# Kernel optimization log

Hardware: AMD Instinct MI355X
Metric: run time of the kernel (lower is better)

Reference implementation:

```python
import jax, jax.numpy as jnp
import numpy as np
from jax import lax

BN_EPS = 1e-5


def _fps(xyz, npoint):
    # Farthest point sampling; deterministic start at index 0 per batch
    # (original uses a random start; the math of the loop is identical).
    B, N, _ = xyz.shape
    init_dist = jnp.full((B, N), 1e10, dtype=xyz.dtype)
    init_far = jnp.zeros((B,), dtype=jnp.int32)

    def step(carry, _):
        dist, far = carry
        centroid = jnp.take_along_axis(xyz, far[:, None, None], axis=1)  # [B,1,3]
        d = jnp.sum((xyz - centroid) ** 2, axis=-1)  # [B,N]
        dist = jnp.minimum(dist, d)
        new_far = jnp.argmax(dist, axis=-1).astype(jnp.int32)
        return (dist, new_far), far

    _, idx = lax.scan(step, (init_dist, init_far), None, length=npoint)
    return jnp.transpose(idx)  # [B, npoint]


def _index_points(points, idx):
    # points [B,N,C], idx [B,...] -> [B,...,C]
    return jax.vmap(lambda p, i: p[i])(points, idx)


def _knn(k, xyz, new_xyz):
    # squared euclidean distances [B,S,N]
    d = (jnp.sum(new_xyz ** 2, -1)[:, :, None]
         + jnp.sum(xyz ** 2, -1)[:, None, :]
         - 2.0 * jnp.einsum('bsc,bnc->bsn', new_xyz, xyz))
    _, idx = lax.top_k(-d, k)  # k smallest distances
    return idx


def _conv_bn_relu(x, w, gamma, beta):
    # 1x1 Conv2d (no bias) + BatchNorm2d (training-mode batch stats) + ReLU
    y = jnp.einsum('oc,bcsk->bosk', w, x)
    mean = jnp.mean(y, axis=(0, 2, 3), keepdims=True)
    var = jnp.var(y, axis=(0, 2, 3), keepdims=True)
    y = (y - mean) * lax.rsqrt(var + BN_EPS)
    y = y * gamma[None, :, None, None] + beta[None, :, None, None]
    return jax.nn.relu(y)


def setup_inputs() -> dict:
    key = jax.random.key(0)
    ks = jax.random.split(key, 5)
    B, N, C = 16, 4096, 128
    xyz = jax.random.normal(ks[0], (B, N, 3), dtype=jnp.float32)
    features = jax.random.normal(ks[1], (B, C, N), dtype=jnp.float32)
    w1 = jax.random.normal(ks[2], (128, C + 3), dtype=jnp.float32) * 0.05
    w2 = jax.random.normal(ks[3], (128, 128), dtype=jnp.float32) * 0.05
    w3 = jax.random.normal(ks[4], (256, 128), dtype=jnp.float32) * 0.05
    return {
        'xyz': xyz, 'features': features,
        'w1': w1, 'g1': jnp.ones(128), 'b1': jnp.zeros(128),
        'w2': w2, 'g2': jnp.ones(128), 'b2': jnp.zeros(128),
        'w3': w3, 'g3': jnp.ones(256), 'b3': jnp.zeros(256),
        'npoint': 1024, 'k': 32,
    }


def reference(xyz, features, w1, g1, b1, w2, g2, b2, w3, g3, b3, npoint, k):
    fps_idx = _fps(xyz, npoint)                     # [B,S]
    new_xyz = _index_points(xyz, fps_idx)           # [B,S,3]
    group_idx = _knn(k, xyz, new_xyz)               # [B,S,K]
    grouped_xyz = _index_points(xyz, group_idx)     # [B,S,K,3]
    gxn = grouped_xyz - new_xyz[:, :, None, :]
    feats = jnp.transpose(features, (0, 2, 1))      # [B,N,C]
    gfeat = _index_points(feats, group_idx)         # [B,S,K,C]
    grouped = jnp.concatenate([gxn, gfeat], axis=-1)  # [B,S,K,3+C]
    x = jnp.transpose(grouped, (0, 3, 1, 2))        # [B,3+C,S,K]
    x = _conv_bn_relu(x, w1, g1, b1)
    x = _conv_bn_relu(x, w2, g2, b2)
    x = _conv_bn_relu(x, w3, g3, b3)
    new_features = jnp.max(x, axis=-1)              # [B,256,S]
    return new_xyz, new_features
```

## Files before the change

### kernel.cpp

```cpp
#include <hip/hip_runtime.h>

#define HB 16
#define HN 4096
#define HS 1024
#define HK 32
#define HC 128

typedef _Float16 half8  __attribute__((ext_vector_type(8)));
typedef _Float16 half4v __attribute__((ext_vector_type(4)));
typedef float    f32x4  __attribute__((ext_vector_type(4)));
typedef float    f32x2  __attribute__((ext_vector_type(2)));
typedef unsigned long long u64;

#define WS_BN      4096u
#define WS_A1H     8192u
#define WS_A2H     49152u
#define WS_A3H     81920u
#define WS_XYZPP   147456u
#define WS_GIDX    1196032u
#define WS_FEATT   3293184u
#define WS_Y1      20070400u

__global__ __launch_bounds__(256) void head_kernel(
    const float* __restrict__ xyz, const float* __restrict__ features,
    const float* __restrict__ w1, const float* __restrict__ w2, const float* __restrict__ w3,
    _Float16* __restrict__ a1h, _Float16* __restrict__ a2h, _Float16* __restrict__ a3h,
    _Float16* __restrict__ featt, float4* __restrict__ xyzpp, float* __restrict__ out)
{
#pragma clang fp contract(off)
  __shared__ union {
    float tbuf[64][65];
    struct {
      float xyzt[HN*3];
      unsigned long long K[2][4];
    } fps;
  } lds;
  const int bid = blockIdx.x;
  const int t = threadIdx.x;

  if (bid < 16) {
    const int b = bid;
    const float* xb = xyz + (size_t)b*HN*3;
    f32x2 pX[8], pY[8], pZ[8], dm[8];
    #pragma unroll
    for (int h = 0; h < 8; ++h) {
      #pragma unroll
      for (int e = 0; e < 2; ++e) {
        int n = t*16 + h*2 + e;
        float x = xb[n*3+0], y = xb[n*3+1], z = xb[n*3+2];
        pX[h][e] = x; pY[h][e] = y; pZ[h][e] = z;
        lds.fps.xyzt[n*3+0] = x; lds.fps.xyzt[n*3+1] = y; lds.fps.xyzt[n*3+2] = z;
      }
      dm[h] = f32x2{1e10f, 1e10f};
    }
    float cx = xb[0], cy = xb[1], cz = xb[2];
    float sc[4][3];
    #pragma unroll
    for (int k = 0; k < 4; ++k) { sc[k][0]=0.0f; sc[k][1]=0.0f; sc[k][2]=0.0f; }
    if (t == 0) { out[(size_t)(b*HS)*3+0] = cx; out[(size_t)(b*HS)*3+1] = cy; out[(size_t)(b*HS)*3+2] = cz; }
    const int wv = t >> 6, l = t & 63;

    for (int i = 1; i < HS; ++i) {
      f32x2 vcx = {cx, cx}, vcy = {cy, cy}, vcz = {cz, cz};
      float pm[8];
      #pragma unroll
      for (int h = 0; h < 8; ++h) {
        f32x2 dx = pX[h] - vcx, dy = pY[h] - vcy, dz = pZ[h] - vcz;
        f32x2 d = ((dx*dx) + (dy*dy)) + (dz*dz);
        f32x2 nd = __builtin_elementwise_min(dm[h], d);
        dm[h] = nd;
        pm[h] = fmaxf(nd[0], nd[1]);
      }
      float q0 = fmaxf(pm[0], pm[1]), q1 = fmaxf(pm[2], pm[3]);
      float q2 = fmaxf(pm[4], pm[5]), q3 = fmaxf(pm[6], pm[7]);
      float mymax = fmaxf(fmaxf(q0, q1), fmaxf(q2, q3));
      int xk = __float_as_int(mymax);
      #define WMAXSTEP(ctrl) { int o_ = __builtin_amdgcn_update_dpp(xk, xk, ctrl, 0xF, 0xF, false); \
        xk = __float_as_int(fmaxf(__int_as_float(xk), __int_as_float(o_))); }
      WMAXSTEP(0x111) WMAXSTEP(0x112) WMAXSTEP(0x114)
      WMAXSTEP(0x118) WMAXSTEP(0x142) WMAXSTEP(0x143)
      #undef WMAXSTEP
      float wmax = __int_as_float(__builtin_amdgcn_readlane(xk, 63));
      unsigned long long msk = __ballot(mymax == wmax);
      int winl = __ffsll(msk) - 1;
      int j = 0;
      #pragma unroll
      for (int h = 7; h >= 0; --h) {
        int e = (dm[h][0] == wmax) ? 0 : 1;
        if (pm[h] == wmax) j = 2*h + e;
      }
      int n_cand = t*16 + j;
      int n_w = __builtin_amdgcn_readlane(n_cand, winl);

      const int p = i & 1;
      if (l == 0) {
        lds.fps.K[p][wv] = ((unsigned long long)__float_as_uint(wmax) << 32)
                         | (unsigned int)(HN-1 - n_w);
      }
      __syncthreads();
      unsigned long long k0 = lds.fps.K[p][0], k1 = lds.fps.K[p][1];
      unsigned long long k2 = lds.fps.K[p][2], k3 = lds.fps.K[p][3];
      unsigned long long ka = (k0 >= k1) ? k0 : k1;
      unsigned long long kb = (k2 >= k3) ? k2 : k3;
      unsigned long long kk = (ka >= kb) ? ka : kb;
      int n_best = HN-1 - (int)(unsigned int)(kk & 0xFFFFFFFFull);
      int off = n_best*3;
      cx = lds.fps.xyzt[off+0];
      cy = lds.fps.xyzt[off+1];
      cz = lds.fps.xyzt[off+2];
      if ((i & 255) == t) {
        int s = i >> 8;
        #pragma unroll
        for (int k = 0; k < 4; ++k)
          if (s == k) { sc[k][0] = cx; sc[k][1] = cy; sc[k][2] = cz; }
      }
    }
    #pragma unroll
    for (int k = 0; k < 4; ++k) {
      int i = k*256 + t;
      if (i >= 1) {
        size_t o3 = (size_t)(b*HS + i)*3;
        out[o3+0] = sc[k][0]; out[o3+1] = sc[k][1]; out[o3+2] = sc[k][2];
      }
    }
  } else if (bid < 16 + 1024) {
    const int tb = bid - 16;
    const int bb = tb >> 6, n0 = (tb & 63) * 64;
    const int wvv = t >> 6, lane = t & 63;
    for (int h = 0; h < 2; ++h) {
      #pragma unroll
      for (int rep = 0; rep < 16; ++rep) {
        int cc = rep*4 + wvv;
        lds.tbuf[cc][lane] = features[((size_t)(bb*HC + h*64 + cc))*HN + n0 + lane];
      }
      __syncthreads();
      #pragma unroll
      for (int rep = 0; rep < 2; ++rep) {
        int item = rep*256 + t;
        int n = item >> 3, cg = (item & 7) * 8;
        half8 v;
        #pragma unroll
        for (int j = 0; j < 8; ++j) v[j] = (_Float16)lds.tbuf[cg + j][n];
        *(half8*)(featt + ((size_t)(bb*HN) + n0 + n) * HC + h*64 + cg) = v;
      }
      __syncthreads();
    }
  } else if (bid < 16 + 1024 + 256) {
    int gi = (bid - 1040)*256 + t;
    const float* p = xyz + (size_t)gi*3;
    float x = p[0], y = p[1], z = p[2];
    float pp = ((x*x) + (y*y)) + (z*z);
    xyzpp[gi] = make_float4(x, y, z, pp);
  } else {
    int wi = (bid - 1296)*256 + t;
    if (wi < 20480) {
      int o = wi / 160, c = wi - o*160;
      float v = 0.0f;
      if (c < 128) v = w1[o*131 + 3 + c];
      else if (c < 131) v = w1[o*131 + (c-128)];
      a1h[wi] = (_Float16)v;
    } else if (wi < 20480 + 16384) {
      a2h[wi - 20480] = (_Float16)w2[wi - 20480];
    } else if (wi < 20480 + 16384 + 32768) {
      a3h[wi - 36864] = (_Float16)w3[wi - 36864];
    }
  }
}

#define LEXLT(d1,i1,d2,i2) ((d1) < (d2) || ((d1) == (d2) && (i1) < (i2)))

__global__ __launch_bounds__(64) void knn_p1(
    const float* __restrict__ newxyz, const float4* __restrict__ xyzpp, u64* __restrict__ keybuf)
{
#pragma clang fp contract(off)
  const int t = threadIdx.x;
  const int blk = blockIdx.x;
  const int b = blk >> 7, rem = blk & 127;
  const int shard = rem >> 4, qg = rem & 15;
  const int q = b*1024 + qg*64 + t;
  float qx = newxyz[(size_t)q*3+0], qy = newxyz[(size_t)q*3+1], qz = newxyz[(size_t)q*3+2];
  float qq = ((qx*qx) + (qy*qy)) + (qz*qz);

  const float INF = __builtin_inff();
  float td[32]; int ti[32];
  #pragma unroll
  for (int j = 0; j < 32; ++j) { td[j] = INF; ti[j] = 0x7FFFFFFF; }
  float root = INF;
  int cnt = 0;

  __shared__ float fdl[32][64];
  __shared__ int   fil[32][64];
  const float4* P = xyzpp + (size_t)b*HN + shard*512;

  auto flush = [&]() {
    float gd[32]; int gi2[32];
    #pragma unroll
    for (int j = 0; j < 32; ++j) {
      gd[j] = fdl[j][t]; gi2[j] = fil[j][t];
      if (j >= cnt) { gd[j] = INF; gi2[j] = 0x7FFFFFFF; }
    }
    cnt = 0;
    #pragma unroll
    for (int k = 2; k <= 32; k <<= 1) {
      #pragma unroll
      for (int j = k >> 1; j > 0; j >>= 1) {
        #pragma unroll
        for (int i = 0; i < 32; ++i) {
          int l = i ^ j;
          if (l > i) {
            bool up = ((i & k) == 0);
            bool sw = up ? LEXLT(gd[l], gi2[l], gd[i], gi2[i])
                         : LEXLT(gd[i], gi2[i], gd[l], gi2[l]);
            if (sw) { float tf = gd[i]; gd[i] = gd[l]; gd[l] = tf;
                      int   ii = gi2[i]; gi2[i] = gi2[l]; gi2[l] = ii; }
          }
        }
      }
    }
    #pragma unroll
    for (int i = 0; i < 32; ++i) {
      float od = gd[31-i]; int oi = gi2[31-i];
      if (LEXLT(od, oi, td[i], ti[i])) { td[i] = od; ti[i] = oi; }
    }
    #pragma unroll
    for (int j = 16; j > 0; j >>= 1) {
      #pragma unroll
      for (int i = 0; i < 32; ++i) {
        if ((i & j) == 0) {
          int l = i | j;
          if (LEXLT(td[l], ti[l], td[i], ti[i])) {
            float tf = td[i]; td[i] = td[l]; td[l] = tf;
            int   ii = ti[i]; ti[i] = ti[l]; ti[l] = ii;
          }
        }
      }
    }
    root = td[31];
  };

  for (int n0 = 0; n0 < 512; n0 += 8) {
    float4 pb[8];
    #pragma unroll
    for (int j = 0; j < 8; ++j) pb[j] = P[n0 + j];
    #pragma unroll
    for (int j = 0; j < 8; ++j) {
      float d = (qq + pb[j].w) - 2.0f*(((qx*pb[j].x) + (qy*pb[j].y)) + (qz*pb[j].z));
      if (d < root) { fdl[cnt][t] = d; fil[cnt][t] = shard*512 + n0 + j; cnt++; }
    }
    if (__ballot(cnt > 24)) flush();
  }
  if (__ballot(cnt > 0)) flush();

  const size_t base = (size_t)(b*16 + qg) * 16384 + (size_t)shard * 2048;
  #pragma unroll
  for (int j = 0; j < 32; ++j) {
    unsigned bits = __float_as_uint(td[j]);
    unsigned s = bits ^ (((unsigned)((int)bits >> 31)) | 0x80000000u);
    keybuf[base + (size_t)j*64 + t] = ((u64)s << 32) | (unsigned)ti[j];
  }
}

__global__ __launch_bounds__(64) void knn_p2(const u64* __restrict__ keybuf, int* __restrict__ gidx)
{
  const int t = threadIdx.x;
  const int g = blockIdx.x;
  const size_t base = (size_t)g * 16384;

  u64 tk[32];
  #pragma unroll
  for (int j = 0; j < 32; ++j) tk[j] = ~0ULL;
  u64 root = ~0ULL;
  int cnt = 0;
  __shared__ u64 fk[32][64];

  auto flush64 = [&]() {
    u64 gd[32];
    #pragma unroll
    for (int j = 0; j < 32; ++j) {
      gd[j] = fk[j][t];
      if (j >= cnt) gd[j] = ~0ULL;
    }
    cnt = 0;
    #pragma unroll
    for (int k = 2; k <= 32; k <<= 1) {
      #pragma unroll
      for (int j = k >> 1; j > 0; j >>= 1) {
        #pragma unroll
        for (int i = 0; i < 32; ++i) {
          int l = i ^ j;
          if (l > i) {
            bool up = ((i & k) == 0);
            bool sw = up ? (gd[l] < gd[i]) : (gd[i] < gd[l]);
            if (sw) { u64 tf = gd[i]; gd[i] = gd[l]; gd[l] = tf; }
          }
        }
      }
    }
    #pragma unroll
    for (int i = 0; i < 32; ++i) {
      u64 od = gd[31-i];
      if (od < tk[i]) tk[i] = od;
    }
    #pragma unroll
    for (int j = 16; j > 0; j >>= 1) {
      #pragma unroll
      for (int i = 0; i < 32; ++i) {
        if ((i & j) == 0) {
          int l = i | j;
          if (tk[l] < tk[i]) { u64 tf = tk[i]; tk[i] = tk[l]; tk[l] = tf; }
        }
      }
    }
    root = tk[31];
  };

  for (int k0 = 0; k0 < 256; k0 += 8) {
    u64 kk[8];
    #pragma unroll
    for (int j = 0; j < 8; ++j) kk[j] = keybuf[base + (size_t)(k0 + j)*64 + t];
    #pragma unroll
    for (int j = 0; j < 8; ++j) {
      if (kk[j] < root) { fk[cnt][t] = kk[j]; cnt++; }
    }
    if (__ballot(cnt > 24)) flush64();
  }
  if (__ballot(cnt > 0)) flush64();

  const int q = g*64 + t;
  #pragma unroll
  for (int j = 0; j < 32; j += 4) {
    int4 v = { (int)(unsigned)tk[j], (int)(unsigned)tk[j+1], (int)(unsigned)tk[j+2], (int)(unsigned)tk[j+3] };
    *(int4*)(gidx + ((size_t)q << 5) + j) = v;
  }
}

template<int MODE>
__global__ __launch_bounds__(256, 2) void conv_kernel(
    const _Float16* __restrict__ A, const _Float16* Bsrc,
    const int* __restrict__ gidx, const float4* __restrict__ xyzpp, const float* __restrict__ newxyz,
    const _Float16* __restrict__ bnA, const _Float16* __restrict__ bnB,
    _Float16* Yout, float* __restrict__ pstat, float* __restrict__ pool)
{
  const int tid = threadIdx.x;
  const int w = tid >> 6, l = tid & 63, ll = l & 15, lh = l >> 4;
  const int colbase = blockIdx.x * 256 + w * 64;
  const int b = colbase >> 15;
  const int AS = (MODE == 1) ? 160 : 128;
  const _Float16* Ap = A + (MODE == 3 ? (size_t)blockIdx.y * 128 * 128 : 0);

  f32x4 acc[8][4] = {};

  half8 bnAv[4], bnBv[4];
  if constexpr (MODE >= 2) {
    #pragma unroll
    for (int c = 0; c < 4; ++c) {
      int k0 = c*32 + lh*8;
      bnAv[c] = *(const half8*)(bnA + k0);
      bnBv[c] = *(const half8*)(bnB + k0);
    }
  }
  int gidxv[4];
  if constexpr (MODE == 1) {
    #pragma unroll
    for (int nf = 0; nf < 4; ++nf) gidxv[nf] = gidx[colbase + nf*16 + ll];
  }

  const int NCH = (MODE == 1) ? 5 : 4;
  #pragma unroll
  for (int c = 0; c < NCH; ++c) {
    half8 a[8];
    #pragma unroll
    for (int mf = 0; mf < 8; ++mf)
      a[mf] = *(const half8*)(Ap + (size_t)(mf*16 + ll)*AS + c*32 + lh*8);
    half8 bfr[4];
    #pragma unroll
    for (int nf = 0; nf < 4; ++nf) {
      if constexpr (MODE == 1) {
        if (c < 4) {
          bfr[nf] = *(const half8*)(Bsrc + ((size_t)(b*HN + gidxv[nf]))*HC + c*32 + lh*8);
        } else {
          half8 z = {};
          if (lh == 0) {
            float4 pw = xyzpp[b*HN + gidxv[nf]];
            int col = colbase + nf*16 + ll;
            int s = (col >> 5) & (HS-1);
            const float* nx = newxyz + (size_t)(b*HS + s)*3;
            z[0] = (_Float16)(pw.x - nx[0]);
            z[1] = (_Float16)(pw.y - nx[1]);
            z[2] = (_Float16)(pw.z - nx[2]);
          }
          bfr[nf] = z;
        }
      } else {
        half8 v = *(const half8*)(Bsrc + ((size_t)(colbase + nf*16 + ll))*HC + c*32 + lh*8);
        v = v * bnAv[c] + bnBv[c];
        half8 hz = {};
        bfr[nf] = __builtin_elementwise_max(v, hz);
      }
    }
    #pragma unroll
    for (int mf = 0; mf < 8; ++mf)
      #pragma unroll
      for (int nf = 0; nf < 4; ++nf)
        acc[mf][nf] = __builtin_amdgcn_mfma_f32_16x16x32_f16(a[mf], bfr[nf], acc[mf][nf], 0, 0, 0);
  }

  __shared__ float bsum[128], bsq[128];
  if (tid < 128) { bsum[tid] = 0.0f; bsq[tid] = 0.0f; }
  __syncthreads();

  #pragma unroll
  for (int mf = 0; mf < 8; ++mf) {
    int ch0 = mf*16 + lh*4;
    if constexpr (MODE != 3) {
      #pragma unroll
      for (int nf = 0; nf < 4; ++nf) {
        int col = colbase + nf*16 + ll;
        half4v hv;
        #pragma unroll
        for (int r = 0; r < 4; ++r) hv[r] = (_Float16)acc[mf][nf][r];
        *(half4v*)(Yout + (size_t)col*HC + ch0) = hv;
      }
    } else {
      #pragma unroll
      for (int g = 0; g < 2; ++g) {
        float mx[4];
        #pragma unroll
        for (int r = 0; r < 4; ++r) mx[r] = fmaxf(acc[mf][2*g][r], acc[mf][2*g+1][r]);
        #pragma unroll
        for (int m = 1; m <= 8; m <<= 1)
          #pragma unroll
          for (int r = 0; r < 4; ++r) mx[r] = fmaxf(mx[r], __shfl_xor(mx[r], m, 64));
        if (ll == 0) {
          int s = ((colbase + g*32) >> 5) & (HS-1);
          int chg = blockIdx.y*128 + ch0;
          #pragma unroll
          for (int r = 0; r < 4; ++r)
            pool[(((size_t)(b*256 + chg + r)) << 10) + s] = mx[r];
        }
      }
    }
    float sv[4] = {0,0,0,0}, qv[4] = {0,0,0,0};
    #pragma unroll
    for (int nf = 0; nf < 4; ++nf)
      #pragma unroll
      for (int r = 0; r < 4; ++r) { float v = acc[mf][nf][r]; sv[r] += v; qv[r] += v*v; }
    #pragma unroll
    for (int m = 1; m <= 8; m <<= 1)
      #pragma unroll
      for (int r = 0; r < 4; ++r) { sv[r] += __shfl_xor(sv[r], m, 64); qv[r] += __shfl_xor(qv[r], m, 64); }
    if (ll == 0) {
      #pragma unroll
      for (int r = 0; r < 4; ++r) { atomicAdd(&bsum[ch0+r], sv[r]); atomicAdd(&bsq[ch0+r], qv[r]); }
    }
  }
  __syncthreads();
  float pv = (tid < 128) ? bsum[tid] : bsq[tid - 128];
  pstat[((size_t)(blockIdx.y * gridDim.x + blockIdx.x)) * 256 + tid] = pv;
}

__global__ __launch_bounds__(256) void fin_kernel(
    const float* __restrict__ pstat, int nblk,
    const float* __restrict__ g, const float* __restrict__ be,
    _Float16* __restrict__ Ah, _Float16* __restrict__ Bh,
    float* __restrict__ Af, float* __restrict__ Bf)
{
  const int ch = blockIdx.x;
  const int y = ch >> 7, c = ch & 127;
  const float* base = pstat + (size_t)y * nblk * 256;
  const int t = threadIdx.x;
  float s = 0.0f, q = 0.0f;
  for (int k = t; k < nblk; k += 256) {
    s += base[(size_t)k*256 + c];
    q += base[(size_t)k*256 + 128 + c];
  }
  #pragma unroll
  for (int m = 1; m < 64; m <<= 1) { s += __shfl_xor(s, m, 64); q += __shfl_xor(q, m, 64); }
  __shared__ float ss[4], sq[4];
  if ((t & 63) == 0) { ss[t >> 6] = s; sq[t >> 6] = q; }
  __syncthreads();
  if (t == 0) {
    s = ((ss[0] + ss[1]) + (ss[2] + ss[3]));
    q = ((sq[0] + sq[1]) + (sq[2] + sq[3]));
    float mean = s * (1.0f/524288.0f);
    float var  = q * (1.0f/524288.0f) - mean*mean;
    float a  = g[ch] * rsqrtf(var + 1e-5f);
    float bb = be[ch] - mean*a;
    if (Ah) { Ah[ch] = (_Float16)a; Bh[ch] = (_Float16)bb; }
    else    { Af[ch] = a; Bf[ch] = bb; }
  }
}

__global__ __launch_bounds__(256) void final_affine(float* __restrict__ outp,
                                                    const float* __restrict__ Af,
                                                    const float* __restrict__ Bf)
{
  int i = blockIdx.x*256 + threadIdx.x;
  float4 v = ((float4*)outp)[i];
  int ch = ((i << 2) >> 10) & 255;
  float a = Af[ch], bb = Bf[ch];
  v.x = fmaxf(v.x*a + bb, 0.0f);
  v.y = fmaxf(v.y*a + bb, 0.0f);
  v.z = fmaxf(v.z*a + bb, 0.0f);
  v.w = fmaxf(v.w*a + bb, 0.0f);
  ((float4*)outp)[i] = v;
}

extern "C" void kernel_launch(void* const* d_in, const int* in_sizes, int n_in,
                              void* d_out, int out_size, void* d_ws, size_t ws_size,
                              hipStream_t stream) {
  const float* xyz      = (const float*)d_in[0];
  const float* features = (const float*)d_in[1];
  const float* w1  = (const float*)d_in[2];
  const float* g1  = (const float*)d_in[3];
  const float* b1v = (const float*)d_in[4];
  const float* w2  = (const float*)d_in[5];
  const float* g2  = (const float*)d_in[6];
  const float* b2v = (const float*)d_in[7];
  const float* w3  = (const float*)d_in[8];
  const float* g3  = (const float*)d_in[9];
  const float* b3v = (const float*)d_in[10];
  float* out = (float*)d_out;
  char* ws = (char*)d_ws;

  _Float16* A1h = (_Float16*)(ws + WS_BN);
  _Float16* B1h = A1h + 128;
  _Float16* A2h = A1h + 256;
  _Float16* B2h = A1h + 384;
  float* a3f = (float*)(ws + WS_BN + 1024);
  float* b3f = a3f + 256;
  _Float16* a1h = (_Float16*)(ws + WS_A1H);
  _Float16* a2h = (_Float16*)(ws + WS_A2H);
  _Float16* a3h = (_Float16*)(ws + WS_A3H);
  float4* xyzpp = (float4*)(ws + WS_XYZPP);
  int* gidx = (int*)(ws + WS_GIDX);
  _Float16* featt = (_Float16*)(ws + WS_FEATT);
  u64* keybuf = (u64*)(ws + WS_Y1);
  _Float16* y1 = (_Float16*)(ws + WS_Y1);
  _Float16* y2 = y1;

  float* p1 = out + 49152;
  float* p2 = (float*)(ws + WS_FEATT);
  float* p3 = (float*)(ws + WS_FEATT + 4194304);

  head_kernel<<<1568, 256, 0, stream>>>(xyz, features, w1, w2, w3,
                                        a1h, a2h, a3h, featt, xyzpp, out);
  knn_p1<<<2048, 64, 0, stream>>>(out, xyzpp, keybuf);
  knn_p2<<<256, 64, 0, stream>>>(keybuf, gidx);

  conv_kernel<1><<<2048, 256, 0, stream>>>(a1h, featt, gidx, xyzpp, out,
                                           nullptr, nullptr, y1, p1, nullptr);
  fin_kernel<<<128, 256, 0, stream>>>(p1, 2048, g1, b1v, A1h, B1h, nullptr, nullptr);

  conv_kernel<2><<<2048, 256, 0, stream>>>(a2h, y1, nullptr, nullptr, nullptr,
                                           A1h, B1h, y2, p2, nullptr);
  fin_kernel<<<128, 256, 0, stream>>>(p2, 2048, g2, b2v, A2h, B2h, nullptr, nullptr);

  conv_kernel<3><<<dim3(2048, 2), 256, 0, stream>>>(a3h, y2, nullptr, nullptr, nullptr,
                                                    A2h, B2h, nullptr, p3, out + 49152);
  fin_kernel<<<256, 256, 0, stream>>>(p3, 2048, g3, b3v, nullptr, nullptr, a3f, b3f);

  final_affine<<<4096, 256, 0, stream>>>(out + 49152, a3f, b3f);
}
```

Baseline: 1.330 ms.

## Retile conv kernels to 32 columns per wave and fuse final affine into finalize

```diff
diff --git a/kernel.cpp b/kernel.cpp
--- a/kernel.cpp
+++ b/kernel.cpp
@@ -335,7 +335,7 @@
 }
 
 template<int MODE>
-__global__ __launch_bounds__(256, 2) void conv_kernel(
+__global__ __launch_bounds__(256, (MODE==3) ? 2 : 3) void conv_kernel(
     const _Float16* __restrict__ A, const _Float16* Bsrc,
     const int* __restrict__ gidx, const float4* __restrict__ xyzpp, const float* __restrict__ newxyz,
     const _Float16* __restrict__ bnA, const _Float16* __restrict__ bnB,
@@ -343,12 +343,15 @@
 {
   const int tid = threadIdx.x;
   const int w = tid >> 6, l = tid & 63, ll = l & 15, lh = l >> 4;
-  const int colbase = blockIdx.x * 256 + w * 64;
+  int blk = blockIdx.x;
+  if constexpr (MODE == 1) blk = (blk & 7) * 512 + (blk >> 3);
+  const int colbase = blk * 128 + w * 32;
   const int b = colbase >> 15;
   const int AS = (MODE == 1) ? 160 : 128;
-  const _Float16* Ap = A + (MODE == 3 ? (size_t)blockIdx.y * 128 * 128 : 0);
-
-  f32x4 acc[8][4] = {};
+  const int MH = (MODE == 3) ? 2 : 1;
+  const int CST = (MODE == 3) ? 256 : 128;
+
+  f32x4 acc[(MODE==3)?2:1][8][2] = {};
 
   half8 bnAv[4], bnBv[4];
   if constexpr (MODE >= 2) {
@@ -359,22 +362,18 @@
       bnBv[c] = *(const half8*)(bnB + k0);
     }
   }
-  int gidxv[4];
+  int gidxv[2];
   if constexpr (MODE == 1) {
     #pragma unroll
-    for (int nf = 0; nf < 4; ++nf) gidxv[nf] = gidx[colbase + nf*16 + ll];
+    for (int nf = 0; nf < 2; ++nf) gidxv[nf] = gidx[colbase + nf*16 + ll];
   }
 
   const int NCH = (MODE == 1) ? 5 : 4;
   #pragma unroll
   for (int c = 0; c < NCH; ++c) {
-    half8 a[8];
-    #pragma unroll
-    for (int mf = 0; mf < 8; ++mf)
-      a[mf] = *(const half8*)(Ap + (size_t)(mf*16 + ll)*AS + c*32 + lh*8);
-    half8 bfr[4];
-    #pragma unroll
-    for (int nf = 0; nf < 4; ++nf) {
+    half8 bfr[2];
+    #pragma unroll
+    for (int nf = 0; nf < 2; ++nf) {
       if constexpr (MODE == 1) {
         if (c < 4) {
           bfr[nf] = *(const half8*)(Bsrc + ((size_t)(b*HN + gidxv[nf]))*HC + c*32 + lh*8);
@@ -399,84 +398,98 @@
       }
     }
     #pragma unroll
-    for (int mf = 0; mf < 8; ++mf)
-      #pragma unroll
-      for (int nf = 0; nf < 4; ++nf)
-        acc[mf][nf] = __builtin_amdgcn_mfma_f32_16x16x32_f16(a[mf], bfr[nf], acc[mf][nf], 0, 0, 0);
-  }
-
-  __shared__ float bsum[128], bsq[128];
-  if (tid < 128) { bsum[tid] = 0.0f; bsq[tid] = 0.0f; }
+    for (int mh = 0; mh < MH; ++mh) {
+      half8 a[8];
+      #pragma unroll
+      for (int mf = 0; mf < 8; ++mf)
+        a[mf] = *(const half8*)(A + (size_t)mh*128*128 + (size_t)(mf*16 + ll)*AS + c*32 + lh*8);
+      #pragma unroll
+      for (int mf = 0; mf < 8; ++mf)
+        #pragma unroll
+        for (int nf = 0; nf < 2; ++nf)
+          acc[mh][mf][nf] = __builtin_amdgcn_mfma_f32_16x16x32_f16(a[mf], bfr[nf], acc[mh][mf][nf], 0, 0, 0);
+    }
+  }
+
+  __shared__ float bsum[(MODE==3)?256:128], bsq[(MODE==3)?256:128];
+  if (tid < CST) { bsum[tid] = 0.0f; bsq[tid] = 0.0f; }
   __syncthreads();
 
   #pragma unroll
-  for (int mf = 0; mf < 8; ++mf) {
-    int ch0 = mf*16 + lh*4;
-    if constexpr (MODE != 3) {
-      #pragma unroll
-      for (int nf = 0; nf < 4; ++nf) {
-        int col = colbase + nf*16 + ll;
-        half4v hv;
-        #pragma unroll
-        for (int r = 0; r < 4; ++r) hv[r] = (_Float16)acc[mf][nf][r];
-        *(half4v*)(Yout + (size_t)col*HC + ch0) = hv;
-      }
-    } else {
-      #pragma unroll
-      for (int g = 0; g < 2; ++g) {
+  for (int mh = 0; mh < MH; ++mh) {
+    #pragma unroll
+    for (int mf = 0; mf < 8; ++mf) {
+      int ch0 = mf*16 + lh*4;
+      if constexpr (MODE != 3) {
+        #pragma unroll
+        for (int nf = 0; nf < 2; ++nf) {
+          int col = colbase + nf*16 + ll;
+          half4v hv;
+          #pragma unroll
+          for (int r = 0; r < 4; ++r) hv[r] = (_Float16)acc[0][mf][nf][r];
+          *(half4v*)(Yout + (size_t)col*HC + ch0) = hv;
+        }
+      } else {
         float mx[4];
         #pragma unroll
-        for (int r = 0; r < 4; ++r) mx[r] = fmaxf(acc[mf][2*g][r], acc[mf][2*g+1][r]);
+        for (int r = 0; r < 4; ++r) mx[r] = fmaxf(acc[mh][mf][0][r], acc[mh][mf][1][r]);
         #pragma unroll
         for (int m = 1; m <= 8; m <<= 1)
           #pragma unroll
           for (int r = 0; r < 4; ++r) mx[r] = fmaxf(mx[r], __shfl_xor(mx[r], m, 64));
         if (ll == 0) {
-          int s = ((colbase + g*32) >> 5) & (HS-1);
-          int chg = blockIdx.y*128 + ch0;
+          int s = (colbase >> 5) & (HS-1);
+          int chg = mh*128 + ch0;
           #pragma unroll
           for (int r = 0; r < 4; ++r)
             pool[(((size_t)(b*256 + chg + r)) << 10) + s] = mx[r];
         }
       }
-    }
-    float sv[4] = {0,0,0,0}, qv[4] = {0,0,0,0};
-    #pragma unroll
-    for (int nf = 0; nf < 4; ++nf)
-      #pragma unroll
-      for (int r = 0; r < 4; ++r) { float v = acc[mf][nf][r]; sv[r] += v; qv[r] += v*v; }
-    #pragma unroll
-    for (int m = 1; m <= 8; m <<= 1)
-      #pragma unroll
-      for (int r = 0; r < 4; ++r) { sv[r] += __shfl_xor(sv[r], m, 64); qv[r] += __shfl_xor(qv[r], m, 64); }
-    if (ll == 0) {
-      #pragma unroll
-      for (int r = 0; r < 4; ++r) { atomicAdd(&bsum[ch0+r], sv[r]); atomicAdd(&bsq[ch0+r], qv[r]); }
+      float sv[4] = {0,0,0,0}, qv[4] = {0,0,0,0};
+      #pragma unroll
+      for (int nf = 0; nf < 2; ++nf)
+        #pragma unroll
+        for (int r = 0; r < 4; ++r) { float v = acc[mh][mf][nf][r]; sv[r] += v; qv[r] += v*v; }
+      #pragma unroll
+      for (int m = 1; m <= 8; m <<= 1)
+        #pragma unroll
+        for (int r = 0; r < 4; ++r) { sv[r] += __shfl_xor(sv[r], m, 64); qv[r] += __shfl_xor(qv[r], m, 64); }
+      if (ll == 0) {
+        #pragma unroll
+        for (int r = 0; r < 4; ++r) {
+          atomicAdd(&bsum[mh*128 + ch0 + r], sv[r]);
+          atomicAdd(&bsq[mh*128 + ch0 + r], qv[r]);
+        }
+      }
     }
   }
   __syncthreads();
-  float pv = (tid < 128) ? bsum[tid] : bsq[tid - 128];
-  pstat[((size_t)(blockIdx.y * gridDim.x + blockIdx.x)) * 256 + tid] = pv;
+  if constexpr (MODE == 3) {
+    pstat[(size_t)blockIdx.x*512 + tid] = bsum[tid];
+    pstat[(size_t)blockIdx.x*512 + 256 + tid] = bsq[tid];
+  } else {
+    float pv = (tid < 128) ? bsum[tid] : bsq[tid - 128];
+    pstat[(size_t)blockIdx.x*256 + tid] = pv;
+  }
 }
 
 __global__ __launch_bounds__(256) void fin_kernel(
-    const float* __restrict__ pstat, int nblk,
+    const float* __restrict__ pstat, int nblk, int C,
     const float* __restrict__ g, const float* __restrict__ be,
     _Float16* __restrict__ Ah, _Float16* __restrict__ Bh,
-    float* __restrict__ Af, float* __restrict__ Bf)
+    float* __restrict__ pool)
 {
   const int ch = blockIdx.x;
-  const int y = ch >> 7, c = ch & 127;
-  const float* base = pstat + (size_t)y * nblk * 256;
   const int t = threadIdx.x;
+  const int row = 2*C;
   float s = 0.0f, q = 0.0f;
   for (int k = t; k < nblk; k += 256) {
-    s += base[(size_t)k*256 + c];
-    q += base[(size_t)k*256 + 128 + c];
+    s += pstat[(size_t)k*row + ch];
+    q += pstat[(size_t)k*row + C + ch];
   }
   #pragma unroll
   for (int m = 1; m < 64; m <<= 1) { s += __shfl_xor(s, m, 64); q += __shfl_xor(q, m, 64); }
-  __shared__ float ss[4], sq[4];
+  __shared__ float ss[4], sq[4], sa, sb;
   if ((t & 63) == 0) { ss[t >> 6] = s; sq[t >> 6] = q; }
   __syncthreads();
   if (t == 0) {
@@ -487,23 +500,21 @@
     float a  = g[ch] * rsqrtf(var + 1e-5f);
     float bb = be[ch] - mean*a;
     if (Ah) { Ah[ch] = (_Float16)a; Bh[ch] = (_Float16)bb; }
-    else    { Af[ch] = a; Bf[ch] = bb; }
-  }
-}
-
-__global__ __launch_bounds__(256) void final_affine(float* __restrict__ outp,
-                                                    const float* __restrict__ Af,
-                                                    const float* __restrict__ Bf)
-{
-  int i = blockIdx.x*256 + threadIdx.x;
-  float4 v = ((float4*)outp)[i];
-  int ch = ((i << 2) >> 10) & 255;
-  float a = Af[ch], bb = Bf[ch];
-  v.x = fmaxf(v.x*a + bb, 0.0f);
-  v.y = fmaxf(v.y*a + bb, 0.0f);
-  v.z = fmaxf(v.z*a + bb, 0.0f);
-  v.w = fmaxf(v.w*a + bb, 0.0f);
-  ((float4*)outp)[i] = v;
+    sa = a; sb = bb;
+  }
+  __syncthreads();
+  if (pool) {
+    float a = sa, bb = sb;
+    for (int bi = 0; bi < 16; ++bi) {
+      float4* p = (float4*)(pool + (((size_t)(bi*256 + ch)) << 10));
+      float4 v = p[t];
+      v.x = fmaxf(v.x*a + bb, 0.0f);
+      v.y = fmaxf(v.y*a + bb, 0.0f);
+      v.z = fmaxf(v.z*a + bb, 0.0f);
+      v.w = fmaxf(v.w*a + bb, 0.0f);
+      p[t] = v;
+    }
+  }
 }
 
 extern "C" void kernel_launch(void* const* d_in, const int* in_sizes, int n_in,
@@ -527,8 +538,6 @@
   _Float16* B1h = A1h + 128;
   _Float16* A2h = A1h + 256;
   _Float16* B2h = A1h + 384;
-  float* a3f = (float*)(ws + WS_BN + 1024);
-  float* b3f = a3f + 256;
   _Float16* a1h = (_Float16*)(ws + WS_A1H);
   _Float16* a2h = (_Float16*)(ws + WS_A2H);
   _Float16* a3h = (_Float16*)(ws + WS_A3H);
@@ -548,17 +557,15 @@
   knn_p1<<<2048, 64, 0, stream>>>(out, xyzpp, keybuf);
   knn_p2<<<256, 64, 0, stream>>>(keybuf, gidx);
 
-  conv_kernel<1><<<2048, 256, 0, stream>>>(a1h, featt, gidx, xyzpp, out,
+  conv_kernel<1><<<4096, 256, 0, stream>>>(a1h, featt, gidx, xyzpp, out,
                                            nullptr, nullptr, y1, p1, nullptr);
-  fin_kernel<<<128, 256, 0, stream>>>(p1, 2048, g1, b1v, A1h, B1h, nullptr, nullptr);
-
-  conv_kernel<2><<<2048, 256, 0, stream>>>(a2h, y1, nullptr, nullptr, nullptr,
+  fin_kernel<<<128, 256, 0, stream>>>(p1, 4096, 128, g1, b1v, A1h, B1h, nullptr);
+
+  conv_kernel<2><<<4096, 256, 0, stream>>>(a2h, y1, nullptr, nullptr, nullptr,
                                            A1h, B1h, y2, p2, nullptr);
-  fin_kernel<<<128, 256, 0, stream>>>(p2, 2048, g2, b2v, A2h, B2h, nullptr, nullptr);
-
-  conv_kernel<3><<<dim3(2048, 2), 256, 0, stream>>>(a3h, y2, nullptr, nullptr, nullptr,
-                                                    A2h, B2h, nullptr, p3, out + 49152);
-  fin_kernel<<<256, 256, 0, stream>>>(p3, 2048, g3, b3v, nullptr, nullptr, a3f, b3f);
-
-  final_affine<<<4096, 256, 0, stream>>>(out + 49152, a3f, b3f);
+  fin_kernel<<<128, 256, 0, stream>>>(p2, 4096, 128, g2, b2v, A2h, B2h, nullptr);
+
+  conv_kernel<3><<<4096, 256, 0, stream>>>(a3h, y2, nullptr, nullptr, nullptr,
+                                           A2h, B2h, nullptr, p3, out + 49152);
+  fin_kernel<<<256, 256, 0, stream>>>(p3, 4096, 256, g3, b3v, nullptr, nullptr, out + 49152);
 }
```

Result: slower. 1.434 ms (+7.8%).
